# Kernel tuning notes

Hardware: AMD Instinct MI355X
Metric: run time of the kernel (lower is better)

## Reference

```python
import jax, jax.numpy as jnp
import numpy as np

B, S, H = 2, 2048, 2048
NH = 16
HD = H // NH  # 128


def setup_inputs() -> dict:
    key = jax.random.key(0)
    ks = jax.random.split(key, 6)
    sc = 0.02
    return {
        "x": jax.random.normal(ks[0], (B, S, H), dtype=jnp.float32),
        "attention_mask": jnp.zeros((B, S), dtype=jnp.float32),
        "Wq": jax.random.normal(ks[1], (H, H), dtype=jnp.float32) * sc,
        "bq": jnp.zeros((H,), dtype=jnp.float32),
        "Wk": jax.random.normal(ks[2], (H, H), dtype=jnp.float32) * sc,
        "bk": jnp.zeros((H,), dtype=jnp.float32),
        "Wv": jax.random.normal(ks[3], (H, H), dtype=jnp.float32) * sc,
        "bv": jnp.zeros((H,), dtype=jnp.float32),
        "Wo": jax.random.normal(ks[4], (H, H), dtype=jnp.float32) * sc,
        "bo": jnp.zeros((H,), dtype=jnp.float32),
    }


def reference(x, attention_mask, Wq, bq, Wk, bk, Wv, bv, Wo, bo):
    b, s, h = x.shape
    q = (x @ Wq + bq).reshape(b, s, NH, HD)
    k = (x @ Wk + bk).reshape(b, s, NH, HD)
    v = (x @ Wv + bv).reshape(b, s, NH, HD)
    scale = 1.0 / jnp.sqrt(jnp.asarray(HD, dtype=x.dtype))
    scores = jnp.einsum('bqhd,bkhd->bhqk', q, k) * scale
    scores = scores + attention_mask[:, None, None, :]
    weights = jax.nn.softmax(scores, axis=-1)
    attn = jnp.einsum('bhqk,bkhd->bqhd', weights, v).reshape(b, s, h)
    return attn @ Wo + bo
```

## Files before the change

kernel.cpp:

```cpp
#include <hip/hip_runtime.h>
#include <hip/hip_bf16.h>
#include <stdint.h>

#define BB   2
#define SS   2048
#define HHH  2048
#define NHH  16
#define HDD  128
#define MTOT 4096

typedef __bf16 bf16x8 __attribute__((ext_vector_type(8)));
typedef float  f32x4  __attribute__((ext_vector_type(4)));
typedef float  f32x16 __attribute__((ext_vector_type(16)));

#define MFMA16(a, b, c) __builtin_amdgcn_mfma_f32_16x16x32_bf16((a), (b), (c), 0, 0, 0)
#define MFMA32(a, b, c) __builtin_amdgcn_mfma_f32_32x32x16_bf16((a), (b), (c), 0, 0, 0)

__device__ __forceinline__ unsigned short f2bf(float f) {
    union { float f; unsigned u; } v; v.f = f;
    unsigned r = v.u + 0x7FFFu + ((v.u >> 16) & 1u);
    return (unsigned short)(r >> 16);
}

__device__ __forceinline__ unsigned packbf(float a, float b) {
    union { __bf16 h[2]; unsigned u; } p;
    p.h[0] = (__bf16)a; p.h[1] = (__bf16)b;
    return p.u;
}

__device__ __forceinline__ void pswap(unsigned &a, unsigned &b) {
    asm("v_permlane32_swap_b32 %0, %1" : "+v"(a), "+v"(b));
}

__device__ __forceinline__ float2 xswap(float x) {
    unsigned a = __builtin_bit_cast(unsigned, x);
    unsigned b;
    asm("v_mov_b32 %0, %1" : "=v"(b) : "v"(a));
    asm("v_permlane32_swap_b32 %0, %1" : "+v"(a), "+v"(b));
    return make_float2(__builtin_bit_cast(float, a), __builtin_bit_cast(float, b));
}

__device__ __forceinline__ void gload16(const void* src, void* lds) {
    __builtin_amdgcn_global_load_lds(
        (__attribute__((address_space(1))) void*)src,
        (__attribute__((address_space(3))) void*)lds,
        16, 0, 0);
}

__global__ void cast_f32_bf16(const float* __restrict__ in,
                              unsigned short* __restrict__ out, int n) {
    int i = (blockIdx.x * blockDim.x + threadIdx.x) * 4;
    int stride = gridDim.x * blockDim.x * 4;
    for (; i < n; i += stride) {
        float4 v = *(const float4*)(in + i);
        ushort4 o;
        o.x = f2bf(v.x); o.y = f2bf(v.y); o.z = f2bf(v.z); o.w = f2bf(v.w);
        *(ushort4*)(out + i) = o;
    }
}

__global__ void transpose_cast(const float* __restrict__ in,
                               unsigned short* __restrict__ out) {
    __shared__ float tile[32][33];
    int c0 = blockIdx.x * 32, r0 = blockIdx.y * 32;
    int tx = threadIdx.x, ty = threadIdx.y;
    #pragma unroll
    for (int i = 0; i < 32; i += 8)
        tile[ty + i][tx] = in[(size_t)(r0 + ty + i) * HHH + c0 + tx];
    __syncthreads();
    #pragma unroll
    for (int i = 0; i < 32; i += 8)
        out[(size_t)(c0 + ty + i) * HHH + r0 + tx] = f2bf(tile[tx][ty + i]);
}

template<int MODE>
__global__ __launch_bounds__(256, 2) void gemm_bf16(
    const unsigned short* __restrict__ A,
    const unsigned short* __restrict__ Bt,
    const float* __restrict__ bias,
    void* __restrict__ Cout,
    int M, int N, int K)
{
    __shared__ __align__(16) unsigned char sm[16384];
    const int tid = threadIdx.x;
    const int wv = tid >> 6, ln = tid & 63;
    const int g = ln >> 4, r = ln & 15;
    const int wr = wv >> 1, wc = wv & 1;
    const int m0 = blockIdx.x * 128, n0 = blockIdx.y * 128;

    size_t srcA[2], srcB[2];
    int ldsA[2], ldsB[2];
    #pragma unroll
    for (int i = 0; i < 2; ++i) {
        int ch = wv * 2 + i;
        int o = ch * 1024 + ln * 16;
        int row = o >> 6;
        int gl = ((o >> 4) & 3) ^ ((row >> 1) & 3);
        ldsA[i] = ch * 1024;
        ldsB[i] = 8192 + ch * 1024;
        srcA[i] = (size_t)(m0 + row) * K + gl * 8;
        srcB[i] = (size_t)(n0 + row) * K + gl * 8;
    }

    f32x4 acc[4][4];
    #pragma unroll
    for (int i = 0; i < 4; ++i)
        #pragma unroll
        for (int j = 0; j < 4; ++j)
            acc[i][j] = (f32x4){0.f, 0.f, 0.f, 0.f};

    for (int kt = 0; kt < K; kt += 32) {
        __syncthreads();
        #pragma unroll
        for (int i = 0; i < 2; ++i) {
            gload16(A + srcA[i] + kt, sm + ldsA[i]);
            gload16(Bt + srcB[i] + kt, sm + ldsB[i]);
        }
        __syncthreads();

        bf16x8 af[4], bfr[4];
        #pragma unroll
        for (int t = 0; t < 4; ++t) {
            int rowa = wr * 64 + t * 16 + r;
            int pha = g ^ ((rowa >> 1) & 3);
            af[t] = *(const bf16x8*)(sm + rowa * 64 + pha * 16);
            int rowb = wc * 64 + t * 16 + r;
            int phb = g ^ ((rowb >> 1) & 3);
            bfr[t] = *(const bf16x8*)(sm + 8192 + rowb * 64 + phb * 16);
        }
        #pragma unroll
        for (int mt = 0; mt < 4; ++mt)
            #pragma unroll
            for (int nt = 0; nt < 4; ++nt)
                acc[mt][nt] = MFMA16(af[mt], bfr[nt], acc[mt][nt]);
    }

    #pragma unroll
    for (int mt = 0; mt < 4; ++mt) {
        #pragma unroll
        for (int nt = 0; nt < 4; ++nt) {
            int col = n0 + wc * 64 + nt * 16 + r;
            float bvv = bias[col];
            f32x4 a = acc[mt][nt];
            int mrow = m0 + wr * 64 + mt * 16 + g * 4;
            if (MODE == 0) {
                #pragma unroll
                for (int q = 0; q < 4; ++q)
                    ((unsigned short*)Cout)[(size_t)(mrow + q) * N + col] = f2bf(a[q] + bvv);
            } else if (MODE == 2) {
                #pragma unroll
                for (int q = 0; q < 4; ++q)
                    ((float*)Cout)[(size_t)(mrow + q) * N + col] = a[q] + bvv;
            } else {
                int b = mrow >> 11, s0x = mrow & 2047;
                ushort4 o;
                o.x = f2bf(a[0] + bvv); o.y = f2bf(a[1] + bvv);
                o.z = f2bf(a[2] + bvv); o.w = f2bf(a[3] + bvv);
                *(ushort4*)((unsigned short*)Cout + ((size_t)(b * 2048 + col)) * 2048 + s0x) = o;
            }
        }
    }
}

__global__ __launch_bounds__(256, 2) void attn_fwd(
    const unsigned short* __restrict__ Q,
    const unsigned short* __restrict__ K,
    const unsigned short* __restrict__ V,
    const float* __restrict__ mask,
    unsigned short* __restrict__ O)
{
    __shared__ __align__(16) unsigned char sm[65536];
    const int tid = threadIdx.x, wv = tid >> 6, ln = tid & 63;
    const int hi = ln >> 5, qr = ln & 31;

    const int bid = blockIdx.x;
    const int lb = (bid & 7) * 64 + (bid >> 3);
    const int qb = lb & 15;
    const int bh = lb >> 4;
    const int h = bh & 15, b = bh >> 4;

    const size_t rowQ0 = (size_t)(b * 2048 + qb * 128 + wv * 32);
    const float SCL2 = 0.08838834764831845f * 1.4426950408889634f;
    const float L2E  = 1.4426950408889634f;

    unsigned srcK[4], srcV[4];
    int ldsK[4], ldsV[4];
    #pragma unroll
    for (int i = 0; i < 4; ++i) {
        int ch = wv * 4 + i;
        int o = ch * 1024 + ln * 16;
        { int row = o >> 8; int gl = ((o >> 4) & 15) ^ (row & 7);
          srcK[i] = (unsigned)((b * 2048 + row) * 2048 + h * 128 + gl * 8);
          ldsK[i] = ch * 1024; }
        { int d = o >> 7; int gl = ((o >> 4) & 7) ^ (d & 7);
          srcV[i] = (unsigned)((b * 2048 + h * 128 + d) * 2048 + gl * 8);
          ldsV[i] = 16384 + ch * 1024; }
    }

    #pragma unroll
    for (int i = 0; i < 4; ++i) {
        gload16(K + srcK[i], sm + ldsK[i]);
        gload16(V + srcV[i], sm + ldsV[i]);
    }

    bf16x8 qf[8];
    #pragma unroll
    for (int ks = 0; ks < 8; ++ks)
        qf[ks] = *(const bf16x8*)(Q + (rowQ0 + qr) * 2048 + h * 128 + ks * 16 + hi * 8);

    f32x16 acc[4];
    #pragma unroll
    for (int i = 0; i < 4; ++i)
        #pragma unroll
        for (int j = 0; j < 16; ++j)
            acc[i][j] = 0.f;
    float mr = -3.0e38f, lr = 0.f;

    const float* mb = mask + b * 2048;
    int cur = 0;
    __syncthreads();

    for (int kb = 0; kb < SS; kb += 64) {
        if (kb + 64 < SS) {
            const unsigned char* dst = sm + (cur ^ 1) * 32768;
            int ko = (kb + 64) * 2048;
            #pragma unroll
            for (int i = 0; i < 4; ++i) {
                gload16(K + srcK[i] + ko, (void*)(dst + ldsK[i]));
                gload16(V + srcV[i] + (kb + 64), (void*)(dst + ldsV[i]));
            }
        }
        const unsigned char* Kt = sm + cur * 32768;
        const unsigned char* Vt = Kt + 16384;

        f32x4 mk[2][4];
        #pragma unroll
        for (int kb2 = 0; kb2 < 2; ++kb2)
            #pragma unroll
            for (int rg = 0; rg < 4; ++rg)
                mk[kb2][rg] = *(const f32x4*)(mb + kb + kb2 * 32 + rg * 8 + hi * 4);

        f32x16 sf0, sf1;
        #pragma unroll
        for (int j = 0; j < 16; ++j) { sf0[j] = 0.f; sf1[j] = 0.f; }
        __builtin_amdgcn_s_setprio(1);
        #pragma unroll
        for (int ks = 0; ks < 8; ++ks) {
            int row0 = qr, row1 = 32 + qr;
            int s0 = ((2 * ks + hi) ^ (row0 & 7));
            int s1 = ((2 * ks + hi) ^ (row1 & 7));
            bf16x8 kf0 = *(const bf16x8*)(Kt + row0 * 256 + s0 * 16);
            bf16x8 kf1 = *(const bf16x8*)(Kt + row1 * 256 + s1 * 16);
            sf0 = MFMA32(kf0, qf[ks], sf0);
            sf1 = MFMA32(kf1, qf[ks], sf1);
        }
        __builtin_amdgcn_s_setprio(0);

        float sv[2][16];
        #pragma unroll
        for (int reg = 0; reg < 16; ++reg) {
            sv[0][reg] = sf0[reg] * SCL2 + mk[0][reg >> 2][reg & 3] * L2E;
            sv[1][reg] = sf1[reg] * SCL2 + mk[1][reg >> 2][reg & 3] * L2E;
        }

        float mx[8];
        #pragma unroll
        for (int j = 0; j < 8; ++j)
            mx[j] = fmaxf(fmaxf(sv[0][2*j], sv[0][2*j+1]),
                          fmaxf(sv[1][2*j], sv[1][2*j+1]));
        float m01 = fmaxf(fmaxf(fmaxf(mx[0], mx[1]), fmaxf(mx[2], mx[3])),
                          fmaxf(fmaxf(mx[4], mx[5]), fmaxf(mx[6], mx[7])));
        float2 mp = xswap(m01);
        float mt = fmaxf(mp.x, mp.y);

        float alpha = 1.f;
        int allskip = __all(mt <= mr + 8.f);
        if (!allskip) {
            float nm = fmaxf(mr, mt);
            alpha = __builtin_amdgcn_exp2f(mr - nm);
            mr = nm;
            #pragma unroll
            for (int dblk = 0; dblk < 4; ++dblk)
                #pragma unroll
                for (int reg = 0; reg < 16; ++reg)
                    acc[dblk][reg] *= alpha;
        }

        float s0 = 0.f, s1 = 0.f, s2 = 0.f, s3 = 0.f;
        #pragma unroll
        for (int kb2 = 0; kb2 < 2; ++kb2)
            #pragma unroll
            for (int reg = 0; reg < 16; reg += 4) {
                float p0 = __builtin_amdgcn_exp2f(sv[kb2][reg + 0] - mr);
                float p1 = __builtin_amdgcn_exp2f(sv[kb2][reg + 1] - mr);
                float p2 = __builtin_amdgcn_exp2f(sv[kb2][reg + 2] - mr);
                float p3 = __builtin_amdgcn_exp2f(sv[kb2][reg + 3] - mr);
                sv[kb2][reg + 0] = p0; sv[kb2][reg + 1] = p1;
                sv[kb2][reg + 2] = p2; sv[kb2][reg + 3] = p3;
                s0 += p0; s1 += p1; s2 += p2; s3 += p3;
            }
        float rsl = (s0 + s1) + (s2 + s3);
        float2 rp = xswap(rsl);
        float rs = rp.x + rp.y;
        lr = lr * alpha + rs;

        bf16x8 pfr[4];
        #pragma unroll
        for (int kb16 = 0; kb16 < 4; ++kb16) {
            const int kb2 = kb16 >> 1, i2 = kb16 & 1;
            float* pv = sv[kb2];
            unsigned W00 = packbf(pv[(2*i2+0)*4 + 0], pv[(2*i2+0)*4 + 1]);
            unsigned W01 = packbf(pv[(2*i2+0)*4 + 2], pv[(2*i2+0)*4 + 3]);
            unsigned W10 = packbf(pv[(2*i2+1)*4 + 0], pv[(2*i2+1)*4 + 1]);
            unsigned W11 = packbf(pv[(2*i2+1)*4 + 2], pv[(2*i2+1)*4 + 3]);
            pswap(W00, W10);
            pswap(W01, W11);
            union { unsigned w[4]; bf16x8 v; } u;
            u.w[0] = W00; u.w[1] = W01; u.w[2] = W10; u.w[3] = W11;
            pfr[kb16] = u.v;
        }

        __builtin_amdgcn_s_setprio(1);
        #pragma unroll
        for (int dblk = 0; dblk < 4; ++dblk) {
            int d = dblk * 32 + qr;
            f32x16 a = acc[dblk];
            #pragma unroll
            for (int kb16 = 0; kb16 < 4; ++kb16) {
                int s = ((2 * kb16 + hi) ^ (d & 7));
                bf16x8 vf = *(const bf16x8*)(Vt + d * 128 + s * 16);
                a = MFMA32(vf, pfr[kb16], a);
            }
            acc[dblk] = a;
        }
        __builtin_amdgcn_s_setprio(0);

        __syncthreads();
        cur ^= 1;
    }

    float linv = 1.f / lr;
    unsigned short* orow = O + (rowQ0 + qr) * 2048 + h * 128;
    #pragma unroll
    for (int dblk = 0; dblk < 4; ++dblk)
        #pragma unroll
        for (int rg = 0; rg < 4; ++rg) {
            float v0 = acc[dblk][rg * 4 + 0] * linv;
            float v1 = acc[dblk][rg * 4 + 1] * linv;
            float v2 = acc[dblk][rg * 4 + 2] * linv;
            float v3 = acc[dblk][rg * 4 + 3] * linv;
            uint2 o;
            o.x = packbf(v0, v1);
            o.y = packbf(v2, v3);
            *(uint2*)(orow + dblk * 32 + rg * 8 + hi * 4) = o;
        }
}

extern "C" void kernel_launch(void* const* d_in, const int* in_sizes, int n_in,
                              void* d_out, int out_size, void* d_ws, size_t ws_size,
                              hipStream_t stream)
{
    (void)in_sizes; (void)n_in; (void)out_size; (void)ws_size;
    const float* x    = (const float*)d_in[0];
    const float* mask = (const float*)d_in[1];
    const float* Wq   = (const float*)d_in[2];
    const float* bq   = (const float*)d_in[3];
    const float* Wk   = (const float*)d_in[4];
    const float* bk   = (const float*)d_in[5];
    const float* Wv   = (const float*)d_in[6];
    const float* bv   = (const float*)d_in[7];
    const float* Wo   = (const float*)d_in[8];
    const float* bo   = (const float*)d_in[9];
    float* out = (float*)d_out;

    char* ws = (char*)d_ws;
    unsigned short* xb  = (unsigned short*)(ws);
    unsigned short* Wqt = (unsigned short*)(ws + (16u << 20));
    unsigned short* Wkt = (unsigned short*)(ws + (24u << 20));
    unsigned short* Wvt = (unsigned short*)(ws + (32u << 20));
    unsigned short* Wot = (unsigned short*)(ws + (40u << 20));
    unsigned short* Qb  = (unsigned short*)(ws + (48u << 20));
    unsigned short* Kb  = (unsigned short*)(ws + (64u << 20));
    unsigned short* Vtb = (unsigned short*)(ws + (80u << 20));
    unsigned short* Ab  = (unsigned short*)(ws + (16u << 20));

    cast_f32_bf16<<<2048, 256, 0, stream>>>(x, xb, MTOT * HHH);
    dim3 tb(32, 8), tg(64, 64);
    transpose_cast<<<tg, tb, 0, stream>>>(Wq, Wqt);
    transpose_cast<<<tg, tb, 0, stream>>>(Wk, Wkt);
    transpose_cast<<<tg, tb, 0, stream>>>(Wv, Wvt);
    transpose_cast<<<tg, tb, 0, stream>>>(Wo, Wot);

    dim3 gg(MTOT / 128, HHH / 128);
    gemm_bf16<0><<<gg, 256, 0, stream>>>(xb, Wqt, bq, Qb,  MTOT, HHH, HHH);
    gemm_bf16<0><<<gg, 256, 0, stream>>>(xb, Wkt, bk, Kb,  MTOT, HHH, HHH);
    gemm_bf16<1><<<gg, 256, 0, stream>>>(xb, Wvt, bv, Vtb, MTOT, HHH, HHH);

    attn_fwd<<<BB * NHH * (SS / 128), 256, 0, stream>>>(Qb, Kb, Vtb, mask, Ab);

    gemm_bf16<2><<<gg, 256, 0, stream>>>(Ab, Wot, bo, out, MTOT, HHH, HHH);
}
```

Baseline: 309.3 us.

## Rewrite projection GEMMs with 8-wave 128x256 tiles and triple-buffered LDS pipeline

```diff
diff --git a/kernel.cpp b/kernel.cpp
--- a/kernel.cpp
+++ b/kernel.cpp
@@ -59,8 +59,11 @@
     }
 }
 
-__global__ void transpose_cast(const float* __restrict__ in,
-                               unsigned short* __restrict__ out) {
+__global__ void transpose_cast4(const float* __restrict__ W0, const float* __restrict__ W1,
+                                const float* __restrict__ W2, const float* __restrict__ W3,
+                                unsigned short* __restrict__ out) {
+    const float* in = blockIdx.z == 0 ? W0 : blockIdx.z == 1 ? W1 : blockIdx.z == 2 ? W2 : W3;
+    unsigned short* o = out + (size_t)blockIdx.z * ((size_t)HHH * HHH);
     __shared__ float tile[32][33];
     int c0 = blockIdx.x * 32, r0 = blockIdx.y * 32;
     int tx = threadIdx.x, ty = threadIdx.y;
@@ -70,36 +73,45 @@
     __syncthreads();
     #pragma unroll
     for (int i = 0; i < 32; i += 8)
-        out[(size_t)(c0 + ty + i) * HHH + r0 + tx] = f2bf(tile[tx][ty + i]);
+        o[(size_t)(c0 + ty + i) * HHH + r0 + tx] = f2bf(tile[tx][ty + i]);
 }
 
 template<int MODE>
-__global__ __launch_bounds__(256, 2) void gemm_bf16(
+__global__ __launch_bounds__(512, 2) void gemm8_bf16(
     const unsigned short* __restrict__ A,
     const unsigned short* __restrict__ Bt,
     const float* __restrict__ bias,
     void* __restrict__ Cout,
     int M, int N, int K)
 {
-    __shared__ __align__(16) unsigned char sm[16384];
+    __shared__ __align__(16) unsigned char sm[147456];
     const int tid = threadIdx.x;
     const int wv = tid >> 6, ln = tid & 63;
     const int g = ln >> 4, r = ln & 15;
-    const int wr = wv >> 1, wc = wv & 1;
-    const int m0 = blockIdx.x * 128, n0 = blockIdx.y * 128;
-
-    size_t srcA[2], srcB[2];
-    int ldsA[2], ldsB[2];
-    #pragma unroll
-    for (int i = 0; i < 2; ++i) {
-        int ch = wv * 2 + i;
-        int o = ch * 1024 + ln * 16;
-        int row = o >> 6;
-        int gl = ((o >> 4) & 3) ^ ((row >> 1) & 3);
-        ldsA[i] = ch * 1024;
-        ldsB[i] = 8192 + ch * 1024;
-        srcA[i] = (size_t)(m0 + row) * K + gl * 8;
-        srcB[i] = (size_t)(n0 + row) * K + gl * 8;
+    const int wr = wv >> 2, wc = wv & 3;
+
+    const int bid = blockIdx.x;
+    const int lb = (bid & 7) * 32 + (bid >> 3);
+    const int m0 = (lb & 31) * 128;
+    const int n0 = (lb >> 5) * 256;
+
+    unsigned srcA[2]; int ldsA[2];
+    #pragma unroll
+    for (int j = 0; j < 2; ++j) {
+        int o = j * 8192 + tid * 16;
+        int row = o >> 7;
+        int lg = ((o >> 4) & 7) ^ (row & 7);
+        srcA[j] = (unsigned)(m0 + row) * K + lg * 8;
+        ldsA[j] = o;
+    }
+    unsigned srcB[4]; int ldsB[4];
+    #pragma unroll
+    for (int j = 0; j < 4; ++j) {
+        int o = j * 8192 + tid * 16;
+        int row = o >> 7;
+        int lg = ((o >> 4) & 7) ^ (row & 7);
+        srcB[j] = (unsigned)(n0 + row) * K + lg * 8;
+        ldsB[j] = 16384 + o;
     }
 
     f32x4 acc[4][4];
@@ -109,30 +121,114 @@
         for (int j = 0; j < 4; ++j)
             acc[i][j] = (f32x4){0.f, 0.f, 0.f, 0.f};
 
-    for (int kt = 0; kt < K; kt += 32) {
-        __syncthreads();
-        #pragma unroll
-        for (int i = 0; i < 2; ++i) {
-            gload16(A + srcA[i] + kt, sm + ldsA[i]);
-            gload16(Bt + srcB[i] + kt, sm + ldsB[i]);
-        }
-        __syncthreads();
-
-        bf16x8 af[4], bfr[4];
-        #pragma unroll
-        for (int t = 0; t < 4; ++t) {
-            int rowa = wr * 64 + t * 16 + r;
-            int pha = g ^ ((rowa >> 1) & 3);
-            af[t] = *(const bf16x8*)(sm + rowa * 64 + pha * 16);
-            int rowb = wc * 64 + t * 16 + r;
-            int phb = g ^ ((rowb >> 1) & 3);
-            bfr[t] = *(const bf16x8*)(sm + 8192 + rowb * 64 + phb * 16);
-        }
-        #pragma unroll
-        for (int mt = 0; mt < 4; ++mt)
-            #pragma unroll
-            for (int nt = 0; nt < 4; ++nt)
-                acc[mt][nt] = MFMA16(af[mt], bfr[nt], acc[mt][nt]);
+    const int NT = K >> 6;
+
+    {
+        unsigned char* b0 = sm;
+        unsigned char* b1 = sm + 49152;
+        #pragma unroll
+        for (int j = 0; j < 2; ++j) gload16(A + srcA[j], b0 + ldsA[j]);
+        #pragma unroll
+        for (int j = 0; j < 4; ++j) gload16(Bt + srcB[j], b0 + ldsB[j]);
+        #pragma unroll
+        for (int j = 0; j < 2; ++j) gload16(A + srcA[j] + 64, b1 + ldsA[j]);
+        #pragma unroll
+        for (int j = 0; j < 4; ++j) gload16(Bt + srcB[j] + 64, b1 + ldsB[j]);
+    }
+    asm volatile("s_waitcnt vmcnt(6)" ::: "memory");
+    __builtin_amdgcn_s_barrier();
+
+    int csel = 0;
+    int psel = 2;
+    for (int t = 0; t < NT; ++t) {
+        const unsigned char* Ab = sm + csel * 49152;
+        const unsigned char* Bb = Ab + 16384;
+        unsigned char* Pb = sm + psel * 49152;
+        const bool pre = (t + 2 < NT);
+        const int ko = (t + 2) * 64;
+
+        bf16x8 af[2][2], bf[2][2];
+        #define LDA(mi, ks) (*(const bf16x8*)(Ab + (wr * 64 + (mi) * 16 + r) * 128 + \
+                             ((((ks) << 2) + g) ^ ((wr * 64 + (mi) * 16 + r) & 7)) * 16))
+        #define LDB(ni, ks) (*(const bf16x8*)(Bb + (wc * 64 + (ni) * 16 + r) * 128 + \
+                             ((((ks) << 2) + g) ^ ((wc * 64 + (ni) * 16 + r) & 7)) * 16))
+
+        af[0][0] = LDA(0, 0); af[0][1] = LDA(0, 1);
+        af[1][0] = LDA(1, 0); af[1][1] = LDA(1, 1);
+        bf[0][0] = LDB(0, 0); bf[0][1] = LDB(0, 1);
+        bf[1][0] = LDB(1, 0); bf[1][1] = LDB(1, 1);
+        if (pre) { gload16(Bt + srcB[0] + ko, Pb + ldsB[0]);
+                   gload16(Bt + srcB[1] + ko, Pb + ldsB[1]); }
+        __builtin_amdgcn_s_barrier();
+        asm volatile("s_waitcnt lgkmcnt(0)" ::: "memory");
+        __builtin_amdgcn_s_setprio(1);
+        #pragma unroll
+        for (int mi = 0; mi < 2; ++mi)
+            #pragma unroll
+            for (int ni = 0; ni < 2; ++ni)
+                #pragma unroll
+                for (int ks = 0; ks < 2; ++ks)
+                    acc[mi][ni] = MFMA16(af[mi][ks], bf[ni][ks], acc[mi][ni]);
+        __builtin_amdgcn_s_setprio(0);
+        __builtin_amdgcn_s_barrier();
+
+        bf[0][0] = LDB(2, 0); bf[0][1] = LDB(2, 1);
+        bf[1][0] = LDB(3, 0); bf[1][1] = LDB(3, 1);
+        if (pre) { gload16(Bt + srcB[2] + ko, Pb + ldsB[2]);
+                   gload16(Bt + srcB[3] + ko, Pb + ldsB[3]); }
+        __builtin_amdgcn_s_barrier();
+        asm volatile("s_waitcnt lgkmcnt(0)" ::: "memory");
+        __builtin_amdgcn_s_setprio(1);
+        #pragma unroll
+        for (int mi = 0; mi < 2; ++mi)
+            #pragma unroll
+            for (int ni = 0; ni < 2; ++ni)
+                #pragma unroll
+                for (int ks = 0; ks < 2; ++ks)
+                    acc[mi][ni + 2] = MFMA16(af[mi][ks], bf[ni][ks], acc[mi][ni + 2]);
+        __builtin_amdgcn_s_setprio(0);
+        __builtin_amdgcn_s_barrier();
+
+        af[0][0] = LDA(2, 0); af[0][1] = LDA(2, 1);
+        af[1][0] = LDA(3, 0); af[1][1] = LDA(3, 1);
+        if (pre) { gload16(A + srcA[0] + ko, Pb + ldsA[0]);
+                   gload16(A + srcA[1] + ko, Pb + ldsA[1]); }
+        __builtin_amdgcn_s_barrier();
+        asm volatile("s_waitcnt lgkmcnt(0)" ::: "memory");
+        __builtin_amdgcn_s_setprio(1);
+        #pragma unroll
+        for (int mi = 0; mi < 2; ++mi)
+            #pragma unroll
+            for (int ni = 0; ni < 2; ++ni)
+                #pragma unroll
+                for (int ks = 0; ks < 2; ++ks)
+                    acc[mi + 2][ni + 2] = MFMA16(af[mi][ks], bf[ni][ks], acc[mi + 2][ni + 2]);
+        __builtin_amdgcn_s_setprio(0);
+        __builtin_amdgcn_s_barrier();
+
+        bf[0][0] = LDB(0, 0); bf[0][1] = LDB(0, 1);
+        bf[1][0] = LDB(1, 0); bf[1][1] = LDB(1, 1);
+        __builtin_amdgcn_s_barrier();
+        asm volatile("s_waitcnt lgkmcnt(0)" ::: "memory");
+        __builtin_amdgcn_s_setprio(1);
+        #pragma unroll
+        for (int mi = 0; mi < 2; ++mi)
+            #pragma unroll
+            for (int ni = 0; ni < 2; ++ni)
+                #pragma unroll
+                for (int ks = 0; ks < 2; ++ks)
+                    acc[mi + 2][ni] = MFMA16(af[mi][ks], bf[ni][ks], acc[mi + 2][ni]);
+        __builtin_amdgcn_s_setprio(0);
+        __builtin_amdgcn_s_barrier();
+
+        if (pre) asm volatile("s_waitcnt vmcnt(6)" ::: "memory");
+        else     asm volatile("s_waitcnt vmcnt(0)" ::: "memory");
+        __builtin_amdgcn_s_barrier();
+
+        csel = (csel == 2) ? 0 : csel + 1;
+        psel = (psel == 2) ? 0 : psel + 1;
+        #undef LDA
+        #undef LDB
     }
 
     #pragma unroll
@@ -385,18 +481,13 @@
     unsigned short* Ab  = (unsigned short*)(ws + (16u << 20));
 
     cast_f32_bf16<<<2048, 256, 0, stream>>>(x, xb, MTOT * HHH);
-    dim3 tb(32, 8), tg(64, 64);
-    transpose_cast<<<tg, tb, 0, stream>>>(Wq, Wqt);
-    transpose_cast<<<tg, tb, 0, stream>>>(Wk, Wkt);
-    transpose_cast<<<tg, tb, 0, stream>>>(Wv, Wvt);
-    transpose_cast<<<tg, tb, 0, stream>>>(Wo, Wot);
-
-    dim3 gg(MTOT / 128, HHH / 128);
-    gemm_bf16<0><<<gg, 256, 0, stream>>>(xb, Wqt, bq, Qb,  MTOT, HHH, HHH);
-    gemm_bf16<0><<<gg, 256, 0, stream>>>(xb, Wkt, bk, Kb,  MTOT, HHH, HHH);
-    gemm_bf16<1><<<gg, 256, 0, stream>>>(xb, Wvt, bv, Vtb, MTOT, HHH, HHH);
+    transpose_cast4<<<dim3(64, 64, 4), dim3(32, 8), 0, stream>>>(Wq, Wk, Wv, Wo, Wqt);
+
+    gemm8_bf16<0><<<256, 512, 0, stream>>>(xb, Wqt, bq, Qb,  MTOT, HHH, HHH);
+    gemm8_bf16<0><<<256, 512, 0, stream>>>(xb, Wkt, bk, Kb,  MTOT, HHH, HHH);
+    gemm8_bf16<1><<<256, 512, 0, stream>>>(xb, Wvt, bv, Vtb, MTOT, HHH, HHH);
 
     attn_fwd<<<BB * NHH * (SS / 128), 256, 0, stream>>>(Qb, Kb, Vtb, mask, Ab);
 
-    gemm_bf16<2><<<gg, 256, 0, stream>>>(Ab, Wot, bo, out, MTOT, HHH, HHH);
-}
+    gemm8_bf16<2><<<256, 512, 0, stream>>>(Ab, Wot, bo, out, MTOT, HHH, HHH);
+}
```

Result: faster. 290.6 us (-6.0%).
